# Optimization experiments

Hardware: AMD Instinct MI355X
Metric: run time of the kernel (lower is better)

## Reference

```python
import jax, jax.numpy as jnp
import numpy as np

N = 8192
NHID = 256

def setup_inputs() -> dict:
    key = jax.random.key(0)
    ks = jax.random.split(key, 9)
    s = 1.0 / np.sqrt(NHID)  # torch Linear default init scale
    return {
        "x1": jax.random.normal(ks[0], (N, NHID), jnp.float32),
        "x2": jax.random.normal(ks[1], (N, NHID), jnp.float32),
        "x3": jax.random.normal(ks[2], (N, NHID), jnp.float32),
        "Wq": jax.random.uniform(ks[3], (NHID, NHID), jnp.float32, -s, s),
        "bq": jax.random.uniform(ks[4], (NHID,), jnp.float32, -s, s),
        "Wk": jax.random.uniform(ks[5], (NHID, NHID), jnp.float32, -s, s),
        "bk": jax.random.uniform(ks[6], (NHID,), jnp.float32, -s, s),
        "Wv": jax.random.uniform(ks[7], (NHID, NHID), jnp.float32, -s, s),
        "bv": jax.random.uniform(ks[8], (NHID,), jnp.float32, -s, s),
    }

def reference(x1, x2, x3, Wq, bq, Wk, bk, Wv, bv):
    # torch.nn.Linear: y = x @ W.T + b
    q = x1 @ Wq.T + bq                      # [N, nhid]
    k = x2 @ Wk.T + bk                      # [N, nhid]
    v = x3 @ Wv.T + bv                      # [N, nhid]
    scores = q @ k.T                        # [N, N], NOTE: unscaled (no 1/sqrt(d))
    attn = jax.nn.softmax(scores, axis=1)   # softmax over keys (dim=1)
    return attn @ v                         # [N, nhid]
```

## Files before the change

### kernel.cpp

```cpp
#include <hip/hip_runtime.h>
#include <stdint.h>

typedef unsigned short u16;
typedef __attribute__((ext_vector_type(8))) short short8;
typedef __attribute__((ext_vector_type(4))) float f32x4;
typedef __attribute__((ext_vector_type(16))) float f32x16;

#define LOG2E 1.4426950408889634f
#define NT 8192
#define DH 256

#define QH     0
#define KH     2097152
#define VTB    4194304
#define OPARTB 6291456
#define MPART_F 11534336
#define LPART_F 11599872

__device__ __forceinline__ u16 f2bf(float f) {
  union { float f; uint32_t u; } c; c.f = f;
  uint32_t u = c.u;
  return (u16)((u + 0x7fffu + ((u >> 16) & 1)) >> 16);
}
__device__ __forceinline__ float bf2f(u16 h) {
  union { uint32_t u; float f; } c; c.u = ((uint32_t)h) << 16;
  return c.f;
}

__device__ __forceinline__ int swz32(int u, int h) {
  return (u & 24) | ((u & 7) ^ (h & 7));
}

__device__ __forceinline__ f32x4 mfma16(short8 a, short8 b, f32x4 c) {
  return __builtin_amdgcn_mfma_f32_16x16x32_bf16(a, b, c, 0, 0, 0);
}
__device__ __forceinline__ f32x16 mfma32(short8 a, short8 b, f32x16 c) {
  return __builtin_amdgcn_mfma_f32_32x32x16_bf16(a, b, c, 0, 0, 0);
}

__device__ __forceinline__ void gl_lds16(const u16* g, u16* l) {
  __builtin_amdgcn_global_load_lds(
      (const __attribute__((address_space(1))) uint32_t*)g,
      (__attribute__((address_space(3))) uint32_t*)l, 16, 0, 0);
}

__device__ __forceinline__ void cvt8(const float* v, short8& vh, short8& vl) {
#pragma unroll
  for (int j = 0; j < 8; j++) {
    u16 hh = f2bf(v[j]);
    vh[j] = (short)hh;
    vl[j] = (short)f2bf(v[j] - bf2f(hh));
  }
}

__global__ __launch_bounds__(256) void k_qkv2(
    const float* __restrict__ x1, const float* __restrict__ x2, const float* __restrict__ x3,
    const float* __restrict__ wqp, const float* __restrict__ bqp,
    const float* __restrict__ wkp, const float* __restrict__ bkp,
    const float* __restrict__ wvp, const float* __restrict__ bvp,
    u16* __restrict__ wsu) {
  __shared__ u16 smem[32768];
  u16* sAh = smem;
  u16* sAl = smem + 8192;
  u16* sBh = smem + 16384;
  u16* sBl = smem + 24576;

  int bid = blockIdx.x, tid = threadIdx.x;
  int lane = tid & 63, wave = tid >> 6;
  int n = lane & 15, quad = lane >> 4;
  int wm = wave >> 1, wn = wave & 1;

#pragma unroll 1
  for (int item = 0; item < 2; item++) {
    const float *Asrc, *Bsrc, *bias; u16* O;
    int rowA0, colBase, ldO, biasRow, nG;
    if (item == 0) {
      if (bid < 256) { Asrc = x1; Bsrc = wqp; bias = bqp; O = wsu + QH; rowA0 = bid * 32; }
      else           { Asrc = x2; Bsrc = wkp; bias = bkp; O = wsu + KH; rowA0 = (bid - 256) * 32; }
      colBase = 0; ldO = 256; biasRow = 0; nG = 8;
    } else {
      Asrc = wvp; Bsrc = x3; bias = bvp; O = wsu + VTB;
      rowA0 = (bid & 7) * 32; colBase = (bid >> 3) * 128; ldO = 8192; biasRow = 1; nG = 4;
    }

    __syncthreads();

#pragma unroll
    for (int i = 0; i < 4; i++) {
      int L = i * 256 + tid, row = L >> 5, u = L & 31;
      const float* p = Asrc + (size_t)(rowA0 + row) * 256 + u * 8;
      f32x4 a = *(const f32x4*)p, c = *(const f32x4*)(p + 4);
      float v[8] = {a[0], a[1], a[2], a[3], c[0], c[1], c[2], c[3]};
      short8 vh, vl; cvt8(v, vh, vl);
      *(short8*)(&sAh[row * 256 + swz32(u, row) * 8]) = vh;
      *(short8*)(&sAl[row * 256 + swz32(u, row) * 8]) = vl;
    }

    f32x4 pf[8];
#pragma unroll
    for (int i = 0; i < 4; i++) {
      int L = i * 256 + tid, row = L >> 5, u = L & 31;
      const float* p = Bsrc + (size_t)(colBase + row) * 256 + u * 8;
      pf[i * 2] = *(const f32x4*)p; pf[i * 2 + 1] = *(const f32x4*)(p + 4);
    }
#pragma unroll
    for (int i = 0; i < 4; i++) {
      int L = i * 256 + tid, row = L >> 5, u = L & 31;
      float v[8] = {pf[i*2][0], pf[i*2][1], pf[i*2][2], pf[i*2][3],
                    pf[i*2+1][0], pf[i*2+1][1], pf[i*2+1][2], pf[i*2+1][3]};
      short8 vh, vl; cvt8(v, vh, vl);
      *(short8*)(&sBh[row * 256 + swz32(u, row) * 8]) = vh;
      *(short8*)(&sBl[row * 256 + swz32(u, row) * 8]) = vl;
    }

#pragma unroll 1
    for (int g = 0; g < nG; g++) {
      __syncthreads();

      if (g + 1 < nG) {
        int b0 = colBase + (g + 1) * 32;
#pragma unroll
        for (int i = 0; i < 4; i++) {
          int L = i * 256 + tid, row = L >> 5, u = L & 31;
          const float* p = Bsrc + (size_t)(b0 + row) * 256 + u * 8;
          pf[i * 2] = *(const f32x4*)p; pf[i * 2 + 1] = *(const f32x4*)(p + 4);
        }
      }

      int colg = colBase + g * 32 + wn * 16 + n;
      f32x4 acc = {0.f, 0.f, 0.f, 0.f};
#pragma unroll
      for (int kk = 0; kk < 8; kk++) {
        int ra = wm * 16 + n, rbB = wn * 16 + n;
        short8 ah = *(const short8*)(&sAh[ra * 256 + swz32(kk * 4 + quad, ra) * 8]);
        short8 al = *(const short8*)(&sAl[ra * 256 + swz32(kk * 4 + quad, ra) * 8]);
        short8 bh = *(const short8*)(&sBh[rbB * 256 + swz32(kk * 4 + quad, rbB) * 8]);
        short8 bl = *(const short8*)(&sBl[rbB * 256 + swz32(kk * 4 + quad, rbB) * 8]);
        acc = mfma16(ah, bh, acc);
        acc = mfma16(ah, bl, acc);
        acc = mfma16(al, bh, acc);
      }

      __syncthreads();
      if (g + 1 < nG) {
#pragma unroll
        for (int i = 0; i < 4; i++) {
          int L = i * 256 + tid, row = L >> 5, u = L & 31;
          float v[8] = {pf[i*2][0], pf[i*2][1], pf[i*2][2], pf[i*2][3],
                        pf[i*2+1][0], pf[i*2+1][1], pf[i*2+1][2], pf[i*2+1][3]};
          short8 vh, vl; cvt8(v, vh, vl);
          *(short8*)(&sBh[row * 256 + swz32(u, row) * 8]) = vh;
          *(short8*)(&sBl[row * 256 + swz32(u, row) * 8]) = vl;
        }
      }

      float bcol = biasRow ? 0.0f : bias[colg];
#pragma unroll
      for (int r = 0; r < 4; r++) {
        int rowg = rowA0 + wm * 16 + quad * 4 + r;
        float bb = biasRow ? bias[rowg] : bcol;
        O[(size_t)rowg * ldO + colg] = f2bf(acc[r] + bb);
      }
    }
  }
}

__global__ __launch_bounds__(256, 2) void k_flash(
    const u16* __restrict__ wsu, u16* __restrict__ opart, float* __restrict__ wsf) {
  __shared__ u16 smem[32768];

  int qb = blockIdx.x >> 3, sp = blockIdx.x & 7;
  int tid = threadIdx.x, lane = tid & 63, wave = tid >> 6;
  int key = lane & 31;
  int h = lane >> 5;
  const u16* Qp = wsu + QH;
  const u16* Kp = wsu + KH;
  const u16* Vp = wsu + VTB;

  int rowQ0 = qb * 128 + wave * 32;

  short8 qf[16];
#pragma unroll
  for (int kk = 0; kk < 16; kk++)
    qf[kk] = *(const short8*)(Qp + (size_t)(rowQ0 + key) * 256 + kk * 16 + h * 8);

  int koff[4];
#pragma unroll
  for (int m = 0; m < 4; m++)
    koff[m] = key * 512 + 16 * ((2 * m + h) ^ (key & 7));
  int voff[2];
#pragma unroll
  for (int c = 0; c < 2; c++)
    voff[c] = key * 64 + 16 * ((2 * c + h) ^ ((key >> 1) & 3));

  int krow0 = wave * 2 + h;
  int kgu = (lane & 24) | ((lane & 7) ^ (krow0 & 7));
  int vd_base = wave * 16 + (lane >> 2);
  int vgu = (lane & 3) ^ ((lane >> 3) & 3);

  int key00 = sp * 1024;

#pragma unroll
  for (int i = 0; i < 4; i++) {
    gl_lds16(Kp + (size_t)(key00 + i * 8 + krow0) * 256 + kgu * 8,
             &smem[i * 2048 + wave * 512]);
  }

  f32x16 o[8];
#pragma unroll
  for (int dt = 0; dt < 8; dt++)
#pragma unroll
    for (int r = 0; r < 16; r++) o[dt][r] = 0.f;
  float negm0 = 0.f, lcur = 0.f;

  union PB { uint32_t u[4]; short8 s8; };
  PB pb0, pb1;
#pragma unroll
  for (int j = 0; j < 4; j++) { pb0.u[j] = 0u; pb1.u[j] = 0u; }

#pragma unroll 1
  for (int it = 0; it < 32; it++) {
    __syncthreads();
    int cur = it & 1;
    const u16* sKc = &smem[cur * 8192];
    if (it + 1 < 32) {
      int k1 = key00 + (it + 1) * 32;
#pragma unroll
      for (int i = 0; i < 4; i++)
        gl_lds16(Kp + (size_t)(k1 + i * 8 + krow0) * 256 + kgu * 8,
                 &smem[(cur ^ 1) * 8192 + i * 2048 + wave * 512]);
    }
    {
      int kv = key00 + it * 32;
#pragma unroll
      for (int i = 0; i < 4; i++)
        gl_lds16(Vp + (size_t)(i * 64 + vd_base) * 8192 + kv + vgu * 8,
                 &smem[16384 + cur * 8192 + i * 2048 + wave * 512]);
    }

    const u16* sVp = (it > 0) ? &smem[16384 + (cur ^ 1) * 8192] : sKc;

    f32x16 s;
#pragma unroll
    for (int r = 0; r < 16; r++) s[r] = 0.f;
    __builtin_amdgcn_s_setprio(1);
#pragma unroll
    for (int kk = 0; kk < 16; kk++) {
      short8 kf = *(const short8*)((const char*)sKc + koff[kk & 3] + 128 * (kk >> 2));
      s = mfma32(kf, qf[kk], s);
    }
#pragma unroll
    for (int dt = 0; dt < 8; dt++) {
      short8 v0 = *(const short8*)((const char*)sVp + voff[0] + dt * 2048);
      o[dt] = mfma32(v0, pb0.s8, o[dt]);
    }
#pragma unroll
    for (int dt = 0; dt < 8; dt++) {
      short8 v1 = *(const short8*)((const char*)sVp + voff[1] + dt * 2048);
      o[dt] = mfma32(v1, pb1.s8, o[dt]);
    }
    __builtin_amdgcn_s_setprio(0);

    if (it == 0) {
      float mv = s[0];
#pragma unroll
      for (int r = 1; r < 16; r++) mv = fmaxf(mv, s[r]);
      mv = fmaxf(mv, __shfl_xor(mv, 32));
      negm0 = -mv * LOG2E;
    }

    uint32_t c8[8];
#pragma unroll
    for (int j = 0; j < 8; j++) {
      float x0 = fminf(fmaf(s[2 * j],     LOG2E, negm0), 110.f);
      float x1 = fminf(fmaf(s[2 * j + 1], LOG2E, negm0), 110.f);
      float p0 = exp2f(x0);
      float p1 = exp2f(x1);
      lcur += p0 + p1;
      asm("v_cvt_pk_bf16_f32 %0, %1, %2" : "=v"(c8[j]) : "v"(p0), "v"(p1));
    }
    uint32_t w0a = c8[0], w2a = c8[2], w1a = c8[1], w3a = c8[3];
    asm("v_permlane32_swap_b32 %0, %1" : "+v"(w0a), "+v"(w2a));
    asm("v_permlane32_swap_b32 %0, %1" : "+v"(w1a), "+v"(w3a));
    uint32_t w0b = c8[4], w2b = c8[6], w1b = c8[5], w3b = c8[7];
    asm("v_permlane32_swap_b32 %0, %1" : "+v"(w0b), "+v"(w2b));
    asm("v_permlane32_swap_b32 %0, %1" : "+v"(w1b), "+v"(w3b));
    pb0.u[0] = w0a; pb0.u[1] = w1a; pb0.u[2] = w2a; pb0.u[3] = w3a;
    pb1.u[0] = w0b; pb1.u[1] = w1b; pb1.u[2] = w2b; pb1.u[3] = w3b;
  }

  __syncthreads();
  {
    const u16* sVp = &smem[16384 + 8192];
    __builtin_amdgcn_s_setprio(1);
#pragma unroll
    for (int dt = 0; dt < 8; dt++) {
      short8 v0 = *(const short8*)((const char*)sVp + voff[0] + dt * 2048);
      o[dt] = mfma32(v0, pb0.s8, o[dt]);
    }
#pragma unroll
    for (int dt = 0; dt < 8; dt++) {
      short8 v1 = *(const short8*)((const char*)sVp + voff[1] + dt * 2048);
      o[dt] = mfma32(v1, pb1.s8, o[dt]);
    }
    __builtin_amdgcn_s_setprio(0);
  }

  lcur += __shfl_xor(lcur, 32);

  __syncthreads();
  u16* tb = &smem[wave * 8192];
#pragma unroll
  for (int dt = 0; dt < 8; dt++)
#pragma unroll
    for (int j = 0; j < 4; j++) {
      uint32_t a, b;
      asm("v_cvt_pk_bf16_f32 %0, %1, %2" : "=v"(a) : "v"(o[dt][4 * j + 0]), "v"(o[dt][4 * j + 1]));
      asm("v_cvt_pk_bf16_f32 %0, %1, %2" : "=v"(b) : "v"(o[dt][4 * j + 2]), "v"(o[dt][4 * j + 3]));
      int u16i = (dt * 4 + j) ^ (key & 7);
      uint2 val; val.x = a; val.y = b;
      *(uint2*)((char*)tb + key * 512 + u16i * 16 + h * 8) = val;
    }
  u16* op = opart + (size_t)sp * (NT * DH);
#pragma unroll
  for (int c2i = 0; c2i < 16; c2i++) {
    int rl = c2i * 2 + h;
    int uu = lane & 31;
    short8 vv = *(const short8*)((const char*)tb + rl * 512 + ((uu ^ (rl & 7)) * 16));
    *(short8*)(op + (size_t)(rowQ0 + rl) * 256 + uu * 8) = vv;
  }

  if (lane < 32) {
    int row = rowQ0 + key;
    wsf[MPART_F + sp * NT + row] = negm0 * -0.6931471805599453f;
    wsf[LPART_F + sp * NT + row] = lcur;
  }
}

__global__ __launch_bounds__(256) void k_combine(
    const u16* __restrict__ opart, const float* __restrict__ wsf, float* __restrict__ out) {
  int gid = blockIdx.x * 256 + threadIdx.x;
  int row = gid >> 6, cg = gid & 63;
  float m[8], l[8];
#pragma unroll
  for (int s = 0; s < 8; s++) {
    m[s] = wsf[MPART_F + s * NT + row];
    l[s] = wsf[LPART_F + s * NT + row];
  }
  float ms = m[0];
#pragma unroll
  for (int s = 1; s < 8; s++) ms = fmaxf(ms, m[s]);
  float denom = 0.f;
  float acc[4] = {0.f, 0.f, 0.f, 0.f};
#pragma unroll
  for (int s = 0; s < 8; s++) {
    float w = exp2f((m[s] - ms) * LOG2E);
    denom += w * l[s];
    const u16* pp = opart + ((size_t)s * NT + row) * 256 + cg * 4;
    uint2 v = *(const uint2*)pp;
    acc[0] += w * bf2f((u16)(v.x & 0xffff));
    acc[1] += w * bf2f((u16)(v.x >> 16));
    acc[2] += w * bf2f((u16)(v.y & 0xffff));
    acc[3] += w * bf2f((u16)(v.y >> 16));
  }
  float inv = 1.0f / denom;
  f32x4 r = {acc[0] * inv, acc[1] * inv, acc[2] * inv, acc[3] * inv};
  *(f32x4*)(out + (size_t)row * 256 + cg * 4) = r;
}

extern "C" void kernel_launch(void* const* d_in, const int* in_sizes, int n_in,
                              void* d_out, int out_size, void* d_ws, size_t ws_size,
                              hipStream_t stream) {
  const float* x1 = (const float*)d_in[0];
  const float* x2 = (const float*)d_in[1];
  const float* x3 = (const float*)d_in[2];
  const float* Wq = (const float*)d_in[3];
  const float* bq = (const float*)d_in[4];
  const float* Wk = (const float*)d_in[5];
  const float* bk = (const float*)d_in[6];
  const float* Wv = (const float*)d_in[7];
  const float* bv = (const float*)d_in[8];
  u16* wsu = (u16*)d_ws;
  float* wsf = (float*)d_ws;
  float* out = (float*)d_out;

  k_qkv2<<<dim3(512), dim3(256), 0, stream>>>(x1, x2, x3, Wq, bq, Wk, bk, Wv, bv, wsu);
  k_flash<<<dim3(512), dim3(256), 0, stream>>>(wsu, wsu + OPARTB, wsf);
  k_combine<<<dim3(2048), dim3(256), 0, stream>>>(wsu + OPARTB, wsf, out);
}
```

Before: 196.9 us.

## Fuse split-KV combine into flash kernel via last-block atomic counter

Adds a per-query-block atomic counter, zeroed in the QKV kernel. The last of the 8 split blocks to finish each query block merges the partial outputs and writes the final result inside the flash kernel. This removes the separate combine launch and its launch gap, but the merge for each query block now runs serially in a single block of 256 threads. It also relies on fences and atomics for cross-block visibility. The fused path is enabled only when the workspace is large enough to hold the counters.

```diff
diff --git a/kernel.cpp b/kernel.cpp
--- a/kernel.cpp
+++ b/kernel.cpp
@@ -16,6 +16,7 @@
 #define OPARTB 6291456
 #define MPART_F 11534336
 #define LPART_F 11599872
+#define CNT_BYTE 46661632
 
 __device__ __forceinline__ u16 f2bf(float f) {
   union { float f; uint32_t u; } c; c.f = f;
@@ -58,7 +59,7 @@
     const float* __restrict__ wqp, const float* __restrict__ bqp,
     const float* __restrict__ wkp, const float* __restrict__ bkp,
     const float* __restrict__ wvp, const float* __restrict__ bvp,
-    u16* __restrict__ wsu) {
+    u16* __restrict__ wsu, unsigned* cnt) {
   __shared__ u16 smem[32768];
   u16* sAh = smem;
   u16* sAl = smem + 8192;
@@ -66,6 +67,7 @@
   u16* sBl = smem + 24576;
 
   int bid = blockIdx.x, tid = threadIdx.x;
+  if (cnt && bid == 0 && tid < 64) cnt[tid] = 0u;
   int lane = tid & 63, wave = tid >> 6;
   int n = lane & 15, quad = lane >> 4;
   int wm = wave >> 1, wn = wave & 1;
@@ -166,7 +168,8 @@
 }
 
 __global__ __launch_bounds__(256, 2) void k_flash(
-    const u16* __restrict__ wsu, u16* __restrict__ opart, float* __restrict__ wsf) {
+    const u16* __restrict__ wsu, u16* __restrict__ opart, float* __restrict__ wsf,
+    unsigned* cnt, float* __restrict__ out, int fuse) {
   __shared__ u16 smem[32768];
 
   int qb = blockIdx.x >> 3, sp = blockIdx.x & 7;
@@ -334,6 +337,51 @@
     int row = rowQ0 + key;
     wsf[MPART_F + sp * NT + row] = negm0 * -0.6931471805599453f;
     wsf[LPART_F + sp * NT + row] = lcur;
+  }
+
+  if (!fuse) return;
+
+  __syncthreads();
+  volatile unsigned* flag = (volatile unsigned*)smem;
+  if (tid == 0) {
+    __threadfence();
+    unsigned old = __hip_atomic_fetch_add(&cnt[qb], 1u, __ATOMIC_ACQ_REL,
+                                          __HIP_MEMORY_SCOPE_AGENT);
+    *flag = (old == 7u) ? 1u : 0u;
+  }
+  __syncthreads();
+  if (*flag) {
+    __threadfence();
+#pragma unroll 1
+    for (int w = 0; w < 32; w++) {
+      int idx = w * 256 + tid;
+      int row = qb * 128 + (idx >> 6), cgc = idx & 63;
+      float m[8], l[8];
+#pragma unroll
+      for (int s = 0; s < 8; s++) {
+        m[s] = wsf[MPART_F + s * NT + row];
+        l[s] = wsf[LPART_F + s * NT + row];
+      }
+      float ms = m[0];
+#pragma unroll
+      for (int s = 1; s < 8; s++) ms = fmaxf(ms, m[s]);
+      float denom = 0.f;
+      float acc[4] = {0.f, 0.f, 0.f, 0.f};
+#pragma unroll
+      for (int s = 0; s < 8; s++) {
+        float wgt = exp2f((m[s] - ms) * LOG2E);
+        denom += wgt * l[s];
+        const u16* pp = opart + ((size_t)s * NT + row) * 256 + cgc * 4;
+        uint2 v = *(const uint2*)pp;
+        acc[0] += wgt * bf2f((u16)(v.x & 0xffff));
+        acc[1] += wgt * bf2f((u16)(v.x >> 16));
+        acc[2] += wgt * bf2f((u16)(v.y & 0xffff));
+        acc[3] += wgt * bf2f((u16)(v.y >> 16));
+      }
+      float inv = 1.0f / denom;
+      f32x4 rv = {acc[0] * inv, acc[1] * inv, acc[2] * inv, acc[3] * inv};
+      *(f32x4*)(out + (size_t)row * 256 + cgc * 4) = rv;
+    }
   }
 }
 
@@ -384,7 +432,11 @@
   float* wsf = (float*)d_ws;
   float* out = (float*)d_out;
 
-  k_qkv2<<<dim3(512), dim3(256), 0, stream>>>(x1, x2, x3, Wq, bq, Wk, bk, Wv, bv, wsu);
-  k_flash<<<dim3(512), dim3(256), 0, stream>>>(wsu, wsu + OPARTB, wsf);
-  k_combine<<<dim3(2048), dim3(256), 0, stream>>>(wsu + OPARTB, wsf, out);
-}
+  int fuse = (ws_size >= (size_t)CNT_BYTE + 64 * sizeof(unsigned)) ? 1 : 0;
+  unsigned* cnt = fuse ? (unsigned*)((char*)d_ws + CNT_BYTE) : (unsigned*)0;
+
+  k_qkv2<<<dim3(512), dim3(256), 0, stream>>>(x1, x2, x3, Wq, bq, Wk, bk, Wv, bv, wsu, cnt);
+  k_flash<<<dim3(512), dim3(256), 0, stream>>>(wsu, wsu + OPARTB, wsf, cnt, out, fuse);
+  if (!fuse)
+    k_combine<<<dim3(2048), dim3(256), 0, stream>>>(wsu + OPARTB, wsf, out);
+}
```

Result: slower. 262.7 us (+33.5%).
